# Kernel tuning notes

Hardware: AMD Instinct MI355X
Metric: run time of the kernel (lower is better)

The kernel has to match this reference:

```python
import jax, jax.numpy as jnp
import numpy as np

DIM = 1024
HEADS = 16
HEAD_DIM = DIM // HEADS
SCALE = HEAD_DIM ** -0.5


def setup_inputs() -> dict:
    key = jax.random.key(0)
    k1, k2, k3, k4 = jax.random.split(key, 4)
    x = jax.random.normal(k1, (2, 2048, DIM), dtype=jnp.float32)
    # nn.Linear(dim, 3*dim, bias=False): weight shape (3*dim, dim), y = x @ W.T
    w_qkv = jax.random.normal(k2, (3 * DIM, DIM), dtype=jnp.float32) * (DIM ** -0.5)
    w_proj = jax.random.normal(k3, (DIM, DIM), dtype=jnp.float32) * (DIM ** -0.5)
    head_w = jnp.ones((HEADS,), dtype=jnp.float32)
    return {"x": x, "w_qkv": w_qkv, "w_proj": w_proj, "head_w": head_w}


def reference(x, w_qkv, w_proj, head_w) -> jnp.ndarray:
    B, N, C = x.shape
    qkv = jnp.einsum("bnc,dc->bnd", x, w_qkv)  # [B,N,3C]
    qkv = qkv.reshape(B, N, 3, HEADS, HEAD_DIM).transpose(2, 0, 3, 1, 4)
    q, k, v = qkv[0], qkv[1], qkv[2]  # each [B,H,N,Dh]
    attn = jnp.einsum("bhqd,bhkd->bhqk", q, k) * SCALE  # [B,H,N,N]
    attn = jax.nn.softmax(attn, axis=-1)
    out = jnp.einsum("bhqk,bhkd->bhqd", attn, v)  # [B,H,N,Dh]
    hw = jax.nn.softmax(head_w)[None, :, None, None]
    out = out * hw
    out = out.transpose(0, 2, 1, 3).reshape(B, N, C)
    return jnp.einsum("bnc,dc->bnd", out, w_proj)
```

## Files before the change

### kernel.cpp

```cpp
#include <hip/hip_runtime.h>

typedef _Float16 half_t;
typedef _Float16 half8 __attribute__((ext_vector_type(8)));
typedef _Float16 half4_t __attribute__((ext_vector_type(4)));
typedef _Float16 half2_t __attribute__((ext_vector_type(2)));
typedef float floatx4 __attribute__((ext_vector_type(4)));
typedef float floatx16 __attribute__((ext_vector_type(16)));

#define B_SZ 2
#define SEQ 2048
#define DIM_ 1024
#define NH 16
#define DH 64
#define ROWS (B_SZ * SEQ)
#define NJS 4

__device__ __forceinline__ void gl2lds16(const void* g, void* l) {
  __builtin_amdgcn_global_load_lds((const __attribute__((address_space(1))) unsigned int*)g,
                                   (__attribute__((address_space(3))) unsigned int*)l, 16, 0, 0);
}

__device__ __forceinline__ float fexp2(float x) {
#if __has_builtin(__builtin_amdgcn_exp2f)
  return __builtin_amdgcn_exp2f(x);
#else
  return __expf(x * 0.6931471805599453f);
#endif
}

__device__ __forceinline__ half4_t pack4(float p0, float p1, float p2, float p3) {
#if __has_builtin(__builtin_amdgcn_cvt_pkrtz)
  half2_t lo = __builtin_bit_cast(half2_t, __builtin_amdgcn_cvt_pkrtz(p0, p1));
  half2_t hi = __builtin_bit_cast(half2_t, __builtin_amdgcn_cvt_pkrtz(p2, p3));
  half4_t r;
  r.x = lo.x; r.y = lo.y; r.z = hi.x; r.w = hi.y;
  return r;
#else
  half4_t r;
  r.x = (half_t)p0; r.y = (half_t)p1; r.z = (half_t)p2; r.w = (half_t)p3;
  return r;
#endif
}

__global__ __launch_bounds__(256) void convert_all(const float4* __restrict__ x,
                                                   const float4* __restrict__ wq,
                                                   const float4* __restrict__ wp,
                                                   half4_t* __restrict__ dst,
                                                   int nx, int nq, int np) {
  int i = blockIdx.x * blockDim.x + threadIdx.x;
  float4 v;
  if (i < nx) v = x[i];
  else if (i < nx + nq) v = wq[i - nx];
  else if (i < nx + nq + np) v = wp[i - nx - nq];
  else return;
  half4_t h;
  h.x = (half_t)v.x; h.y = (half_t)v.y; h.z = (half_t)v.z; h.w = (half_t)v.w;
  dst[i] = h;
}

template <int MODE, int BN>
__global__ __launch_bounds__(256) void gemm32(const half_t* __restrict__ A,
                                              const half_t* __restrict__ Bt,
                                              half_t* __restrict__ q16,
                                              half_t* __restrict__ k16,
                                              half_t* __restrict__ vT16,
                                              float* __restrict__ outp) {
  constexpr int K = 1024;
  constexpr int NT = BN / 64;
  __shared__ __align__(16) half_t a_lds[128 * 64];
  __shared__ __align__(16) half_t b_lds[BN * 64];
  const int t = threadIdx.x;
  const int wave = t >> 6, lane = t & 63;
  const int l31 = lane & 31, hw = lane >> 5;
  const int wm = wave >> 1, wn = wave & 1;
  const int row0 = blockIdx.y * 128, col0 = blockIdx.x * BN;

  floatx16 acc[2][NT];
#pragma unroll
  for (int i = 0; i < 2; ++i)
#pragma unroll
    for (int j = 0; j < NT; ++j)
#pragma unroll
      for (int r = 0; r < 16; ++r) acc[i][j][r] = 0.f;

  for (int k0 = 0; k0 < K; k0 += 64) {
#pragma unroll
    for (int hi = 0; hi < 4; ++hi) {
      int s = t + hi * 256;
      int row = s >> 3, c = s & 7;
      int sc = c ^ (row & 7);
      gl2lds16(A + (size_t)(row0 + row) * K + (k0 + sc * 8), a_lds + (wave * 64 + hi * 256) * 8);
    }
#pragma unroll
    for (int hi = 0; hi < BN / 32; ++hi) {
      int s = t + hi * 256;
      int row = s >> 3, c = s & 7;
      int sc = c ^ (row & 7);
      gl2lds16(Bt + (size_t)(col0 + row) * K + (k0 + sc * 8), b_lds + (wave * 64 + hi * 256) * 8);
    }
    __syncthreads();
    half8 af[2][4], bf[NT][4];
#pragma unroll
    for (int mt = 0; mt < 2; ++mt) {
      int row = wm * 64 + mt * 32 + l31;
#pragma unroll
      for (int kf = 0; kf < 4; ++kf)
        af[mt][kf] = *(const half8*)(a_lds + row * 64 + ((kf * 2 + hw) ^ (row & 7)) * 8);
    }
#pragma unroll
    for (int nt = 0; nt < NT; ++nt) {
      int row = wn * (BN / 2) + nt * 32 + l31;
#pragma unroll
      for (int kf = 0; kf < 4; ++kf)
        bf[nt][kf] = *(const half8*)(b_lds + row * 64 + ((kf * 2 + hw) ^ (row & 7)) * 8);
    }
#pragma unroll
    for (int kf = 0; kf < 4; ++kf)
#pragma unroll
      for (int mt = 0; mt < 2; ++mt)
#pragma unroll
        for (int nt = 0; nt < NT; ++nt)
          acc[mt][nt] =
              __builtin_amdgcn_mfma_f32_32x32x16_f16(af[mt][kf], bf[nt][kf], acc[mt][nt], 0, 0, 0);
    __syncthreads();
  }

  if (MODE == 0) {
    const int which = col0 >> 10;
#pragma unroll
    for (int mt = 0; mt < 2; ++mt)
#pragma unroll
      for (int nt = 0; nt < NT; ++nt) {
        int growb = row0 + wm * 64 + mt * 32;
        int gcol = col0 + wn * (BN / 2) + nt * 32 + l31;
        int hc = gcol & 1023, h = hc >> 6, d = hc & 63;
        if (which == 2) {
#pragma unroll
          for (int rq = 0; rq < 4; ++rq) {
            int grow = growb + 8 * rq + 4 * hw;
            int b = grow >> 11, n0 = grow & 2047;
            int bh = b * NH + h;
            half4_t h4;
            h4.x = (half_t)acc[mt][nt][rq * 4 + 0];
            h4.y = (half_t)acc[mt][nt][rq * 4 + 1];
            h4.z = (half_t)acc[mt][nt][rq * 4 + 2];
            h4.w = (half_t)acc[mt][nt][rq * 4 + 3];
            *(half4_t*)(vT16 + ((size_t)bh * DH + d) * SEQ + n0) = h4;
          }
        } else {
#pragma unroll
          for (int r = 0; r < 16; ++r) {
            int grow = growb + (r & 3) + 8 * (r >> 2) + 4 * hw;
            int b = grow >> 11, n = grow & 2047;
            int bh = b * NH + h;
            float v = acc[mt][nt][r];
            if (which == 0)
              q16[((size_t)bh * SEQ + n) * DH + d] =
                  (half_t)(v * 0.1803368801111204f);
            else
              k16[((size_t)bh * SEQ + n) * DH + d] = (half_t)v;
          }
        }
      }
  } else {
#pragma unroll
    for (int mt = 0; mt < 2; ++mt)
#pragma unroll
      for (int nt = 0; nt < NT; ++nt) {
        int growb = row0 + wm * 64 + mt * 32;
        int gcol = col0 + wn * (BN / 2) + nt * 32 + l31;
#pragma unroll
        for (int r = 0; r < 16; ++r) {
          int grow = growb + (r & 3) + 8 * (r >> 2) + 4 * hw;
          outp[(size_t)grow * DIM_ + gcol] = acc[mt][nt][r];
        }
      }
  }
}

__global__ __launch_bounds__(256) void attn_p1(const half_t* __restrict__ q16,
                                               const half_t* __restrict__ k16,
                                               const half_t* __restrict__ vT16,
                                               half_t* __restrict__ opart,
                                               float* __restrict__ psums) {
  __shared__ __align__(16) half_t k_lds[2][64 * 64];
  __shared__ __align__(16) half_t v_lds[2][64 * 64];

  const int t = threadIdx.x;
  const int wave = t >> 6, lane = t & 63;
  const int l15 = lane & 15, quad = lane >> 4;
  const int blk = blockIdx.x;
  const int js = blk & (NJS - 1), qt = (blk >> 2) & 7, bh = blk >> 5;
  const half_t* qp = q16 + (size_t)bh * SEQ * DH;
  const half_t* kp = k16 + (size_t)bh * SEQ * DH;
  const half_t* vp = vT16 + (size_t)bh * DH * SEQ;
  const int q0w = qt * 256 + wave * 64;
  const int jbase = js * (SEQ / NJS);
  constexpr int NJT = (SEQ / NJS) / 64;

  const int s0 = t, s1 = t + 256;
  const int r0_ = s0 >> 3, c0_ = (s0 & 7) ^ (r0_ & 7);
  const int r1_ = s1 >> 3, c1_ = (s1 & 7) ^ (r1_ & 7);

  half8 qf[4][2];
#pragma unroll
  for (int mi = 0; mi < 4; ++mi)
#pragma unroll
    for (int kf = 0; kf < 2; ++kf)
      qf[mi][kf] = *(const half8*)(qp + (size_t)(q0w + mi * 16 + l15) * DH + kf * 32 + quad * 8);

  const floatx4 z4 = {0.f, 0.f, 0.f, 0.f};
  floatx4 o[4][4];
  floatx4 oex[4];
#pragma unroll
  for (int mi = 0; mi < 4; ++mi) {
    oex[mi] = z4;
#pragma unroll
    for (int i = 0; i < 4; ++i) o[mi][i] = z4;
  }
  half4_t vones;
  vones.x = (half_t)1.f; vones.y = (half_t)1.f; vones.z = (half_t)1.f; vones.w = (half_t)1.f;

  gl2lds16(kp + (size_t)(jbase + r0_) * DH + c0_ * 8, &k_lds[0][(wave * 64) * 8]);
  gl2lds16(vp + (size_t)r0_ * SEQ + jbase + c0_ * 8, &v_lds[0][(wave * 64) * 8]);
  gl2lds16(kp + (size_t)(jbase + r1_) * DH + c1_ * 8, &k_lds[0][(wave * 64 + 256) * 8]);
  gl2lds16(vp + (size_t)r1_ * SEQ + jbase + c1_ * 8, &v_lds[0][(wave * 64 + 256) * 8]);

  int cur = 0;
  for (int jt = 0; jt < NJT; ++jt) {
    __syncthreads();

    if (jt + 1 < NJT) {
      const int j0 = jbase + (jt + 1) * 64, nb = cur ^ 1;
      gl2lds16(kp + (size_t)(j0 + r0_) * DH + c0_ * 8, &k_lds[nb][(wave * 64) * 8]);
      gl2lds16(vp + (size_t)r0_ * SEQ + j0 + c0_ * 8, &v_lds[nb][(wave * 64) * 8]);
      gl2lds16(kp + (size_t)(j0 + r1_) * DH + c1_ * 8, &k_lds[nb][(wave * 64 + 256) * 8]);
      gl2lds16(vp + (size_t)r1_ * SEQ + j0 + c1_ * 8, &v_lds[nb][(wave * 64 + 256) * 8]);
    }

    const half_t* kl = k_lds[cur];
    const half_t* vl = v_lds[cur];

    half4_t pf[4][4];
#pragma unroll
    for (int nt = 0; nt < 4; ++nt) {
      const int row = nt * 16 + l15;
      half8 kb0 = *(const half8*)(kl + row * 64 + ((0 | quad) ^ (row & 7)) * 8);
      half8 kb1 = *(const half8*)(kl + row * 64 + ((4 | quad) ^ (row & 7)) * 8);
      floatx4 st[4];
      __builtin_amdgcn_s_setprio(1);
#pragma unroll
      for (int mi = 0; mi < 4; ++mi)
        st[mi] = __builtin_amdgcn_mfma_f32_16x16x32_f16(kb0, qf[mi][0], z4, 0, 0, 0);
#pragma unroll
      for (int mi = 0; mi < 4; ++mi)
        st[mi] = __builtin_amdgcn_mfma_f32_16x16x32_f16(kb1, qf[mi][1], st[mi], 0, 0, 0);
      __builtin_amdgcn_s_setprio(0);
#pragma unroll
      for (int mi = 0; mi < 4; ++mi) {
        float p0 = fexp2(st[mi][0]);
        float p1 = fexp2(st[mi][1]);
        float p2 = fexp2(st[mi][2]);
        float p3 = fexp2(st[mi][3]);
        pf[mi][nt] = pack4(p0, p1, p2, p3);
      }
    }

    __builtin_amdgcn_s_setprio(1);
#pragma unroll
    for (int jt2 = 0; jt2 < 4; ++jt2) {
#pragma unroll
      for (int dt = 0; dt < 4; ++dt) {
        int row = dt * 16 + l15;
        int ch = (jt2 * 2 + (quad >> 1)) ^ (l15 & 7);
        half4_t vb = *(const half4_t*)(vl + row * 64 + ch * 8 + (quad & 1) * 4);
#pragma unroll
        for (int mi = 0; mi < 4; ++mi)
          o[mi][dt] = __builtin_amdgcn_mfma_f32_16x16x16f16(pf[mi][jt2], vb, o[mi][dt], 0, 0, 0);
      }
#pragma unroll
      for (int mi = 0; mi < 4; ++mi)
        oex[mi] = __builtin_amdgcn_mfma_f32_16x16x16f16(pf[mi][jt2], vones, oex[mi], 0, 0, 0);
    }
    __builtin_amdgcn_s_setprio(0);
    cur ^= 1;
  }

  if (l15 == 0) {
#pragma unroll
    for (int mi = 0; mi < 4; ++mi)
#pragma unroll
      for (int r = 0; r < 4; ++r)
        psums[((size_t)(js * 32 + bh)) * SEQ + q0w + mi * 16 + quad * 4 + r] = oex[mi][r];
  }

#pragma unroll
  for (int mi = 0; mi < 4; ++mi)
#pragma unroll
    for (int r = 0; r < 4; ++r) {
      int n = q0w + mi * 16 + quad * 4 + r;
      size_t base = ((size_t)(js * 32 + bh) * SEQ + n) * DH;
#pragma unroll
      for (int dt = 0; dt < 4; ++dt)
        opart[base + dt * 16 + l15] = (half_t)o[mi][dt][r];
    }
}

__global__ __launch_bounds__(256) void combine(const half_t* __restrict__ opart,
                                               const float* __restrict__ psums,
                                               const float* __restrict__ head_w,
                                               half_t* __restrict__ attn16) {
  int idx = blockIdx.x * blockDim.x + threadIdx.x;
  int d4 = idx & 15, n = (idx >> 4) & 2047, bh = idx >> 15;
  int h = bh & 15, b = bh >> 4;
  const size_t jstr = (size_t)32 * SEQ * DH;
  size_t off = ((size_t)bh * SEQ + n) * DH + d4 * 4;

  float sx = 0.f, sy = 0.f, sz = 0.f, sw2 = 0.f, ps = 0.f;
#pragma unroll
  for (int js = 0; js < NJS; ++js) {
    half4_t ov = *(const half4_t*)(opart + js * jstr + off);
    sx += (float)ov.x; sy += (float)ov.y; sz += (float)ov.z; sw2 += (float)ov.w;
    ps += psums[(size_t)js * 32 * SEQ + (size_t)bh * SEQ + n];
  }

  float mw = head_w[0];
#pragma unroll
  for (int i = 1; i < NH; ++i) mw = fmaxf(mw, head_w[i]);
  float sw = 0.f;
#pragma unroll
  for (int i = 0; i < NH; ++i) sw += __expf(head_w[i] - mw);
  float hwv = __expf(head_w[h] - mw) / sw;

  float scl = hwv / ps;
  half4_t r;
  r.x = (half_t)(sx * scl);
  r.y = (half_t)(sy * scl);
  r.z = (half_t)(sz * scl);
  r.w = (half_t)(sw2 * scl);
  *(half4_t*)(attn16 + ((size_t)(b * SEQ + n)) * DIM_ + h * DH + d4 * 4) = r;
}

extern "C" void kernel_launch(void* const* d_in, const int* in_sizes, int n_in,
                              void* d_out, int out_size, void* d_ws, size_t ws_size,
                              hipStream_t stream) {
  const float* x = (const float*)d_in[0];
  const float* w_qkv = (const float*)d_in[1];
  const float* w_proj = (const float*)d_in[2];
  const float* head_w = (const float*)d_in[3];
  float* out = (float*)d_out;

  half_t* x16 = (half_t*)d_ws;
  half_t* wq16 = x16 + (size_t)ROWS * DIM_;
  half_t* wp16 = wq16 + (size_t)3 * DIM_ * DIM_;
  half_t* q16 = wp16 + (size_t)DIM_ * DIM_;
  half_t* k16 = q16 + (size_t)ROWS * DIM_;
  half_t* vT16 = k16 + (size_t)ROWS * DIM_;
  half_t* attn16 = vT16 + (size_t)ROWS * DIM_;
  half_t* opart = attn16 + (size_t)ROWS * DIM_;
  float* psums = (float*)(opart + (size_t)NJS * 32 * SEQ * DH);

  const int nx = ROWS * DIM_ / 4, nq = 3 * DIM_ * DIM_ / 4, np = DIM_ * DIM_ / 4;
  convert_all<<<(nx + nq + np) / 256, 256, 0, stream>>>((const float4*)x, (const float4*)w_qkv,
                                                        (const float4*)w_proj, (half4_t*)x16,
                                                        nx, nq, np);

  gemm32<0, 128><<<dim3(24, 32), 256, 0, stream>>>(x16, wq16, q16, k16, vT16, nullptr);
  attn_p1<<<32 * 8 * NJS, 256, 0, stream>>>(q16, k16, vT16, opart, psums);
  combine<<<(32 * SEQ * DH / 4) / 256, 256, 0, stream>>>(opart, psums, head_w, attn16);
  gemm32<1, 64><<<dim3(16, 32), 256, 0, stream>>>(attn16, wp16, nullptr, nullptr, nullptr, out);
}
```

Measured before the change: 191.5 us.

## Rewrite attention inner loop with 32x32 MFMA tiles and register row sums

Switches the attention kernel from 16x16 MFMA tiles to 32x32x16 tiles, with each wave handling 32 query rows instead of 64. The softmax denominator is now accumulated in registers from the exp values rather than through an extra MFMA against a ones vector. The key split drops from 4 to 2 while the number of query tiles doubles, so the grid size stays the same. The intent is fewer MFMA instructions per FLOP, no wasted row-sum MFMAs, less partial-output traffic to the combine step, and an occupancy hint of 3 blocks per CU. In exchange, each block runs a longer serial key loop.

Result: no change. 189.5 us (-1.1%).

```diff
diff --git a/kernel.cpp b/kernel.cpp
--- a/kernel.cpp
+++ b/kernel.cpp
@@ -6,6 +6,7 @@
 typedef _Float16 half2_t __attribute__((ext_vector_type(2)));
 typedef float floatx4 __attribute__((ext_vector_type(4)));
 typedef float floatx16 __attribute__((ext_vector_type(16)));
+typedef unsigned int uint4v __attribute__((ext_vector_type(4)));
 
 #define B_SZ 2
 #define SEQ 2048
@@ -13,7 +14,7 @@
 #define NH 16
 #define DH 64
 #define ROWS (B_SZ * SEQ)
-#define NJS 4
+#define NJS 2
 
 __device__ __forceinline__ void gl2lds16(const void* g, void* l) {
   __builtin_amdgcn_global_load_lds((const __attribute__((address_space(1))) unsigned int*)g,
@@ -28,18 +29,23 @@
 #endif
 }
 
-__device__ __forceinline__ half4_t pack4(float p0, float p1, float p2, float p3) {
+__device__ __forceinline__ unsigned cvtpk_u32(float a, float b) {
 #if __has_builtin(__builtin_amdgcn_cvt_pkrtz)
-  half2_t lo = __builtin_bit_cast(half2_t, __builtin_amdgcn_cvt_pkrtz(p0, p1));
-  half2_t hi = __builtin_bit_cast(half2_t, __builtin_amdgcn_cvt_pkrtz(p2, p3));
-  half4_t r;
-  r.x = lo.x; r.y = lo.y; r.z = hi.x; r.w = hi.y;
-  return r;
+  return __builtin_bit_cast(unsigned, __builtin_amdgcn_cvt_pkrtz(a, b));
 #else
-  half4_t r;
-  r.x = (half_t)p0; r.y = (half_t)p1; r.z = (half_t)p2; r.w = (half_t)p3;
-  return r;
+  half2_t h; h.x = (half_t)a; h.y = (half_t)b;
+  return __builtin_bit_cast(unsigned, h);
 #endif
+}
+
+__device__ __forceinline__ half8 pack8(float p0, float p1, float p2, float p3,
+                                       float p4, float p5, float p6, float p7) {
+  uint4v u;
+  u.x = cvtpk_u32(p0, p1);
+  u.y = cvtpk_u32(p2, p3);
+  u.z = cvtpk_u32(p4, p5);
+  u.w = cvtpk_u32(p6, p7);
+  return __builtin_bit_cast(half8, u);
 }
 
 __global__ __launch_bounds__(256) void convert_all(const float4* __restrict__ x,
@@ -178,23 +184,23 @@
   }
 }
 
-__global__ __launch_bounds__(256) void attn_p1(const half_t* __restrict__ q16,
-                                               const half_t* __restrict__ k16,
-                                               const half_t* __restrict__ vT16,
-                                               half_t* __restrict__ opart,
-                                               float* __restrict__ psums) {
+__global__ __launch_bounds__(256, 3) void attn_p1(const half_t* __restrict__ q16,
+                                                  const half_t* __restrict__ k16,
+                                                  const half_t* __restrict__ vT16,
+                                                  half_t* __restrict__ opart,
+                                                  float* __restrict__ psums) {
   __shared__ __align__(16) half_t k_lds[2][64 * 64];
   __shared__ __align__(16) half_t v_lds[2][64 * 64];
 
   const int t = threadIdx.x;
   const int wave = t >> 6, lane = t & 63;
-  const int l15 = lane & 15, quad = lane >> 4;
+  const int l31 = lane & 31, hw = lane >> 5;
   const int blk = blockIdx.x;
-  const int js = blk & (NJS - 1), qt = (blk >> 2) & 7, bh = blk >> 5;
+  const int js = blk & (NJS - 1), qt = (blk >> 1) & 15, bh = blk >> 5;
   const half_t* qp = q16 + (size_t)bh * SEQ * DH;
   const half_t* kp = k16 + (size_t)bh * SEQ * DH;
   const half_t* vp = vT16 + (size_t)bh * DH * SEQ;
-  const int q0w = qt * 256 + wave * 64;
+  const int q0w = qt * 128 + wave * 32;
   const int jbase = js * (SEQ / NJS);
   constexpr int NJT = (SEQ / NJS) / 64;
 
@@ -202,24 +208,17 @@
   const int r0_ = s0 >> 3, c0_ = (s0 & 7) ^ (r0_ & 7);
   const int r1_ = s1 >> 3, c1_ = (s1 & 7) ^ (r1_ & 7);
 
-  half8 qf[4][2];
-#pragma unroll
-  for (int mi = 0; mi < 4; ++mi)
-#pragma unroll
-    for (int kf = 0; kf < 2; ++kf)
-      qf[mi][kf] = *(const half8*)(qp + (size_t)(q0w + mi * 16 + l15) * DH + kf * 32 + quad * 8);
-
-  const floatx4 z4 = {0.f, 0.f, 0.f, 0.f};
-  floatx4 o[4][4];
-  floatx4 oex[4];
-#pragma unroll
-  for (int mi = 0; mi < 4; ++mi) {
-    oex[mi] = z4;
-#pragma unroll
-    for (int i = 0; i < 4; ++i) o[mi][i] = z4;
-  }
-  half4_t vones;
-  vones.x = (half_t)1.f; vones.y = (half_t)1.f; vones.z = (half_t)1.f; vones.w = (half_t)1.f;
+  half8 qf[4];
+#pragma unroll
+  for (int kf = 0; kf < 4; ++kf)
+    qf[kf] = *(const half8*)(qp + (size_t)(q0w + l31) * DH + kf * 16 + hw * 8);
+
+  floatx16 o[2];
+#pragma unroll
+  for (int i = 0; i < 2; ++i)
+#pragma unroll
+    for (int r = 0; r < 16; ++r) o[i][r] = 0.f;
+  float psum = 0.f;
 
   gl2lds16(kp + (size_t)(jbase + r0_) * DH + c0_ * 8, &k_lds[0][(wave * 64) * 8]);
   gl2lds16(vp + (size_t)r0_ * SEQ + jbase + c0_ * 8, &v_lds[0][(wave * 64) * 8]);
@@ -241,68 +240,64 @@
     const half_t* kl = k_lds[cur];
     const half_t* vl = v_lds[cur];
 
-    half4_t pf[4][4];
-#pragma unroll
-    for (int nt = 0; nt < 4; ++nt) {
-      const int row = nt * 16 + l15;
-      half8 kb0 = *(const half8*)(kl + row * 64 + ((0 | quad) ^ (row & 7)) * 8);
-      half8 kb1 = *(const half8*)(kl + row * 64 + ((4 | quad) ^ (row & 7)) * 8);
-      floatx4 st[4];
-      __builtin_amdgcn_s_setprio(1);
-#pragma unroll
-      for (int mi = 0; mi < 4; ++mi)
-        st[mi] = __builtin_amdgcn_mfma_f32_16x16x32_f16(kb0, qf[mi][0], z4, 0, 0, 0);
-#pragma unroll
-      for (int mi = 0; mi < 4; ++mi)
-        st[mi] = __builtin_amdgcn_mfma_f32_16x16x32_f16(kb1, qf[mi][1], st[mi], 0, 0, 0);
-      __builtin_amdgcn_s_setprio(0);
-#pragma unroll
-      for (int mi = 0; mi < 4; ++mi) {
-        float p0 = fexp2(st[mi][0]);
-        float p1 = fexp2(st[mi][1]);
-        float p2 = fexp2(st[mi][2]);
-        float p3 = fexp2(st[mi][3]);
-        pf[mi][nt] = pack4(p0, p1, p2, p3);
+    floatx16 st[2];
+#pragma unroll
+    for (int m = 0; m < 2; ++m)
+#pragma unroll
+      for (int r = 0; r < 16; ++r) st[m][r] = 0.f;
+    __builtin_amdgcn_s_setprio(1);
+#pragma unroll
+    for (int kf = 0; kf < 4; ++kf)
+#pragma unroll
+      for (int m = 0; m < 2; ++m) {
+        int row = m * 32 + l31;
+        half8 kb = *(const half8*)(kl + row * 64 + ((kf * 2 + hw) ^ (row & 7)) * 8);
+        st[m] = __builtin_amdgcn_mfma_f32_32x32x16_f16(kb, qf[kf], st[m], 0, 0, 0);
       }
+    __builtin_amdgcn_s_setprio(0);
+
+    half8 pa[2][2];
+#pragma unroll
+    for (int m = 0; m < 2; ++m) {
+      float p[16];
+#pragma unroll
+      for (int r = 0; r < 16; ++r) p[r] = fexp2(st[m][r]);
+      float a0 = (p[0] + p[1]) + (p[2] + p[3]);
+      float a1 = (p[4] + p[5]) + (p[6] + p[7]);
+      float a2 = (p[8] + p[9]) + (p[10] + p[11]);
+      float a3 = (p[12] + p[13]) + (p[14] + p[15]);
+      psum += (a0 + a1) + (a2 + a3);
+      pa[m][0] = pack8(p[0], p[1], p[2], p[3], p[4], p[5], p[6], p[7]);
+      pa[m][1] = pack8(p[8], p[9], p[10], p[11], p[12], p[13], p[14], p[15]);
     }
 
     __builtin_amdgcn_s_setprio(1);
 #pragma unroll
-    for (int jt2 = 0; jt2 < 4; ++jt2) {
-#pragma unroll
-      for (int dt = 0; dt < 4; ++dt) {
-        int row = dt * 16 + l15;
-        int ch = (jt2 * 2 + (quad >> 1)) ^ (l15 & 7);
-        half4_t vb = *(const half4_t*)(vl + row * 64 + ch * 8 + (quad & 1) * 4);
-#pragma unroll
-        for (int mi = 0; mi < 4; ++mi)
-          o[mi][dt] = __builtin_amdgcn_mfma_f32_16x16x16f16(pf[mi][jt2], vb, o[mi][dt], 0, 0, 0);
+    for (int s = 0; s < 4; ++s) {
+#pragma unroll
+      for (int dt = 0; dt < 2; ++dt) {
+        int row = dt * 32 + l31;
+        int ca = ((s * 2 + 0) ^ (row & 7));
+        int cb = ((s * 2 + 1) ^ (row & 7));
+        half4_t va = *(const half4_t*)(vl + row * 64 + ca * 8 + hw * 4);
+        half4_t vb = *(const half4_t*)(vl + row * 64 + cb * 8 + hw * 4);
+        half8 v8 = __builtin_shufflevector(va, vb, 0, 1, 2, 3, 4, 5, 6, 7);
+        o[dt] = __builtin_amdgcn_mfma_f32_32x32x16_f16(pa[s >> 1][s & 1], v8, o[dt], 0, 0, 0);
       }
-#pragma unroll
-      for (int mi = 0; mi < 4; ++mi)
-        oex[mi] = __builtin_amdgcn_mfma_f32_16x16x16f16(pf[mi][jt2], vones, oex[mi], 0, 0, 0);
     }
     __builtin_amdgcn_s_setprio(0);
     cur ^= 1;
   }
 
-  if (l15 == 0) {
-#pragma unroll
-    for (int mi = 0; mi < 4; ++mi)
-#pragma unroll
-      for (int r = 0; r < 4; ++r)
-        psums[((size_t)(js * 32 + bh)) * SEQ + q0w + mi * 16 + quad * 4 + r] = oex[mi][r];
-  }
-
-#pragma unroll
-  for (int mi = 0; mi < 4; ++mi)
-#pragma unroll
-    for (int r = 0; r < 4; ++r) {
-      int n = q0w + mi * 16 + quad * 4 + r;
-      size_t base = ((size_t)(js * 32 + bh) * SEQ + n) * DH;
-#pragma unroll
-      for (int dt = 0; dt < 4; ++dt)
-        opart[base + dt * 16 + l15] = (half_t)o[mi][dt][r];
+  psum += __shfl_xor(psum, 32, 64);
+  if (hw == 0) psums[((size_t)(js * 32 + bh)) * SEQ + q0w + l31] = psum;
+
+#pragma unroll
+  for (int dt = 0; dt < 2; ++dt)
+#pragma unroll
+    for (int r = 0; r < 16; ++r) {
+      int n = q0w + (r & 3) + 8 * (r >> 2) + 4 * hw;
+      opart[((size_t)(js * 32 + bh) * SEQ + n) * DH + dt * 32 + l31] = (half_t)o[dt][r];
     }
 }
 
@@ -366,7 +361,7 @@
                                                         nx, nq, np);
 
   gemm32<0, 128><<<dim3(24, 32), 256, 0, stream>>>(x16, wq16, q16, k16, vT16, nullptr);
-  attn_p1<<<32 * 8 * NJS, 256, 0, stream>>>(q16, k16, vT16, opart, psums);
+  attn_p1<<<32 * 16 * NJS, 256, 0, stream>>>(q16, k16, vT16, opart, psums);
   combine<<<(32 * SEQ * DH / 4) / 256, 256, 0, stream>>>(opart, psums, head_w, attn16);
   gemm32<1, 64><<<dim3(16, 32), 256, 0, stream>>>(attn16, wp16, nullptr, nullptr, nullptr, out);
 }
```
